# Kernel tuning notes

Measured on AMD Instinct MI355X. Metric: run time of the kernel, lower is better.

## Reference

```python
import jax, jax.numpy as jnp
import numpy as np

N = 100000      # number of nodes
FT = 256        # ft_in (hidden units)
NB_CLASSES = 16 # nb_classes
EPS = 1e-8      # torch.cosine_similarity eps


def setup_inputs() -> dict:
    key = jax.random.key(0)
    ks = jax.random.split(key, 7)
    seq = jax.random.normal(ks[0], (N, FT), dtype=jnp.float32)
    seq1 = jax.random.normal(ks[1], (N, FT), dtype=jnp.float32)
    labels = jax.random.randint(ks[2], (N,), 0, NB_CLASSES, dtype=jnp.int32)
    prompt1 = jax.random.normal(ks[3], (1, FT), dtype=jnp.float32)
    prompt2 = jax.random.normal(ks[4], (1, FT), dtype=jnp.float32)
    prompt3 = jax.random.normal(ks[5], (1, FT), dtype=jnp.float32)
    # weighted_prompt.reset_parameters: fixed init 0.5, 0.4, 0.3
    w_wp = jnp.array([[0.5, 0.4, 0.3]], dtype=jnp.float32)
    # weighted_feature.reset_parameters: fixed init 0.0, 1.0
    w_wf = jnp.array([[0.0, 1.0]], dtype=jnp.float32)
    # downstreamprompt.weight: xavier_uniform on [1, ft_in]
    bound = float(np.sqrt(6.0 / (1 + FT)))
    w_dp = jax.random.uniform(ks[6], (1, FT), jnp.float32, -bound, bound)
    a4 = jnp.array([0.1], dtype=jnp.float32)
    return {"seq": seq, "seq1": seq1, "labels": labels,
            "prompt1": prompt1, "prompt2": prompt2, "prompt3": prompt3,
            "w_wp": w_wp, "w_wf": w_wf, "w_dp": w_dp, "a4": a4}


def reference(seq, seq1, labels, prompt1, prompt2, prompt3, w_wp, w_wf, w_dp, a4):
    # weight = 1 + ELU(weighted_prompt(prompt))  -> [1, FT]
    prompt = jnp.concatenate([prompt1, prompt2, prompt3], axis=0)  # [3, FT]
    weight = 1.0 + jax.nn.elu(w_wp @ prompt)                       # [1, FT]
    rawret1 = weight * seq                                          # [N, FT]
    rawret2 = w_dp * seq                                            # downstreamprompt
    rawret3 = jax.nn.elu(w_wf[0, 0] * rawret1 + w_wf[0, 1] * rawret2)
    rawret = rawret3 + a4[0] * seq1                                 # [N, FT]
    # averageemb (train=1 path): per-class mean, zero-count classes stay 0
    sums = jax.ops.segment_sum(rawret, labels, num_segments=NB_CLASSES)  # [C, FT]
    counts = jax.ops.segment_sum(jnp.ones((rawret.shape[0],), rawret.dtype),
                                 labels, num_segments=NB_CLASSES)        # [C]
    ave = jnp.where(counts[:, None] > 0, sums / jnp.maximum(counts, 1.0)[:, None], sums)
    # fused per-pair cosine similarity: normalize + matmul (replaces N*C loop)
    num = rawret @ ave.T                                             # [N, C]
    denom = (jnp.linalg.norm(rawret, axis=1)[:, None] *
             jnp.linalg.norm(ave, axis=1)[None, :])
    ret = num / jnp.maximum(denom, EPS)
    return jax.nn.softmax(ret, axis=1)
```

## Files before the change

kernel.cpp:

```cpp
#include <hip/hip_runtime.h>
#include <hip/hip_bf16.h>

#define NROWS 100000
#define FT 256
#define NC 16
#define NBLK 512
#define NSL 8
#define SLICE (NBLK / NSL)

#define FPSCALE 1048576.0f
#define FPINV   (1.0f / 1048576.0f)

#define CW_AVEB 0
#define CW_NRM  2048
#define CW_PCNT 2064
#define CW_ST2C (CW_PCNT + NBLK*NC)
#define CW_ST2  (CW_ST2C + NSL*NC)
#define CW_PART (CW_ST2 + NSL*NC*FT)
#define CW_RAWB (CW_PART + NBLK*NC*FT)
#define CW_TOTAL (CW_RAWB + (NROWS*FT)/2)
#define CACHED_NEED_BYTES ((size_t)CW_TOTAL * 4)

#define WS_COEF 0
#define WS_SUMS 256
#define WS_CNTS 4352
#define WS_AVEB 4368
#define WS_NRM  6416

typedef float f32x4 __attribute__((ext_vector_type(4)));
typedef short bf16x8 __attribute__((ext_vector_type(8)));

static __device__ __forceinline__ float bfbits2f(unsigned int u16) {
    union { unsigned int i; float f; } v; v.i = u16 << 16; return v.f;
}
static __device__ __forceinline__ unsigned short f2bf(float f) {
    union { float f; unsigned int i; } v; v.f = f;
    unsigned int u = v.i;
    u += 0x7fffu + ((u >> 16) & 1u);
    return (unsigned short)(u >> 16);
}


__global__ __launch_bounds__(512) void k_accum_c(
    const float* __restrict__ seq,
    const float* __restrict__ seq1,
    const int* __restrict__ labels,
    const float* __restrict__ p1,
    const float* __restrict__ p2,
    const float* __restrict__ p3,
    const float* __restrict__ wwp,
    const float* __restrict__ wwf,
    const float* __restrict__ wdp,
    const float* __restrict__ a4p,
    float* __restrict__ ws)
{
    __shared__ int lsum[NC * FT];
    __shared__ int lcnt[NC];
    __shared__ __align__(16) float scoef[FT];
    const int tid = threadIdx.x;
    for (int i = tid; i < NC * FT; i += 512) lsum[i] = 0;
    if (tid < NC) lcnt[tid] = 0;
    if (tid < FT) {
        float z = wwp[0] * p1[tid] + wwp[1] * p2[tid] + wwp[2] * p3[tid];
        float w = (z > 0.f) ? (1.f + z) : __expf(z);
        scoef[tid] = wwf[0] * w + wwf[1] * wdp[tid];
    }
    __syncthreads();

    const int rr = tid >> 5;
    const int m  = tid & 31;
    const int f0 = m * 8;
    const int mh = m >> 2;
    int off[8];
#pragma unroll
    for (int i = 0; i < 8; ++i) off[i] = (i + mh) & 7;

    float cof[8];
    {
        const float4 c0 = *(const float4*)(scoef + f0);
        const float4 c1 = *(const float4*)(scoef + f0 + 4);
        cof[0]=c0.x; cof[1]=c0.y; cof[2]=c0.z; cof[3]=c0.w;
        cof[4]=c1.x; cof[5]=c1.y; cof[6]=c1.z; cof[7]=c1.w;
    }
    const float a4v = a4p[0];
    unsigned int* rawb = (unsigned int*)(ws + CW_RAWB);

    const int stride = NBLK * 16;
    for (int rowA = blockIdx.x * 16 + rr; rowA < NROWS; rowA += stride * 2) {
        const int rowBr = rowA + stride;
        const bool vB = rowBr < NROWS;
        const int rowB = vB ? rowBr : rowA;
        const int labA = labels[rowA];
        const int labB = labels[rowB];
        const float4 saA = *(const float4*)(seq  + rowA * FT + f0);
        const float4 sbA = *(const float4*)(seq  + rowA * FT + f0 + 4);
        const float4 taA = *(const float4*)(seq1 + rowA * FT + f0);
        const float4 tbA = *(const float4*)(seq1 + rowA * FT + f0 + 4);
        const float4 saB = *(const float4*)(seq  + rowB * FT + f0);
        const float4 sbB = *(const float4*)(seq  + rowB * FT + f0 + 4);
        const float4 taB = *(const float4*)(seq1 + rowB * FT + f0);
        const float4 tbB = *(const float4*)(seq1 + rowB * FT + f0 + 4);

        const float sA[8] = {saA.x,saA.y,saA.z,saA.w, sbA.x,sbA.y,sbA.z,sbA.w};
        const float tA[8] = {taA.x,taA.y,taA.z,taA.w, tbA.x,tbA.y,tbA.z,tbA.w};
        const float sB[8] = {saB.x,saB.y,saB.z,saB.w, sbB.x,sbB.y,sbB.z,sbB.w};
        const float tB[8] = {taB.x,taB.y,taB.z,taB.w, tbB.x,tbB.y,tbB.z,tbB.w};

        int* baseA = lsum + labA * FT + f0;
        unsigned short vbA[8];
#pragma unroll
        for (int i = 0; i < 8; ++i) {
            float u = cof[i] * sA[i];
            float r = (u > 0.f) ? u : (__expf(u) - 1.f);
            float v = r + a4v * tA[i];
            vbA[i] = f2bf(v);
            atomicAdd(baseA + off[i], __float2int_rn(v * FPSCALE));
        }
        uint4 pkA;
        pkA.x = (unsigned int)vbA[0] | ((unsigned int)vbA[1] << 16);
        pkA.y = (unsigned int)vbA[2] | ((unsigned int)vbA[3] << 16);
        pkA.z = (unsigned int)vbA[4] | ((unsigned int)vbA[5] << 16);
        pkA.w = (unsigned int)vbA[6] | ((unsigned int)vbA[7] << 16);
        *(uint4*)(rawb + (rowA * FT + f0) / 2) = pkA;
        if (m == 0) atomicAdd(&lcnt[labA], 1);

        int* baseB = lsum + labB * FT + f0;
        unsigned short vbB[8];
        float vv[8];
#pragma unroll
        for (int i = 0; i < 8; ++i) {
            float u = cof[i] * sB[i];
            float r = (u > 0.f) ? u : (__expf(u) - 1.f);
            vv[i] = r + a4v * tB[i];
            vbB[i] = f2bf(vv[i]);
        }
        if (vB) {
#pragma unroll
            for (int i = 0; i < 8; ++i)
                atomicAdd(baseB + off[i], __float2int_rn(vv[i] * FPSCALE));
            uint4 pkB;
            pkB.x = (unsigned int)vbB[0] | ((unsigned int)vbB[1] << 16);
            pkB.y = (unsigned int)vbB[2] | ((unsigned int)vbB[3] << 16);
            pkB.z = (unsigned int)vbB[4] | ((unsigned int)vbB[5] << 16);
            pkB.w = (unsigned int)vbB[6] | ((unsigned int)vbB[7] << 16);
            *(uint4*)(rawb + (rowB * FT + f0) / 2) = pkB;
            if (m == 0) atomicAdd(&lcnt[labB], 1);
        }
    }
    __syncthreads();

    int* gpart = (int*)(ws + CW_PART) + blockIdx.x * (NC * FT);
    for (int idx = tid; idx < NC * FT; idx += 512) {
        int p  = idx & 255;
        int mm = p >> 3;
        int r  = p & 7;
        int f  = (p & ~7) | ((r - (mm >> 2)) & 7);
        gpart[(idx & ~255) + f] = lsum[idx];
    }
    if (tid < NC) ((int*)(ws + CW_PCNT))[blockIdx.x * NC + tid] = lcnt[tid];
}

__global__ __launch_bounds__(256) void k_reduce1(float* __restrict__ ws)
{
    const int c = blockIdx.x >> 3;
    const int r = blockIdx.x & 7;
    const int f = threadIdx.x;
    const int p0 = r * SLICE;
    const int* gpart = (const int*)(ws + CW_PART);
    int acc = 0;
#pragma unroll 8
    for (int p = 0; p < SLICE; ++p)
        acc += gpart[(p0 + p) * (NC * FT) + c * FT + f];
    ((int*)(ws + CW_ST2))[(r * NC + c) * FT + f] = acc;

    if (f < SLICE) {
        int cc = ((const int*)(ws + CW_PCNT))[(p0 + f) * NC + c];
#pragma unroll
        for (int o = 32; o > 0; o >>= 1) cc += __shfl_down(cc, o, 64);
        if (f == 0) ((int*)(ws + CW_ST2C))[r * NC + c] = cc;
    }
}

__global__ __launch_bounds__(256) void k_reduce2(float* __restrict__ ws)
{
    __shared__ float red[256];
    const int c = blockIdx.x;
    const int f = threadIdx.x;
    const int* st2  = (const int*)(ws + CW_ST2);
    const int* st2c = (const int*)(ws + CW_ST2C);
    long long isum = 0;
    int cnt = 0;
#pragma unroll
    for (int s = 0; s < NSL; ++s) {
        isum += (long long)st2[(s * NC + c) * FT + f];
        cnt  += st2c[s * NC + c];
    }
    float a = ((float)isum * FPINV) / fmaxf((float)cnt, 1.f);
    unsigned short ab = f2bf(a);
    ((unsigned short*)(ws + CW_AVEB))[c * FT + f] = ab;
    float af = bfbits2f(ab);

    red[f] = af * af;
    __syncthreads();
#pragma unroll
    for (int s = 128; s > 0; s >>= 1) {
        if (f < s) red[f] += red[f + s];
        __syncthreads();
    }
    if (f == 0) ws[CW_NRM + c] = sqrtf(red[0]);
}

__global__ __launch_bounds__(256) void k_out_c(
    const float* __restrict__ ws,
    float* __restrict__ out)
{
    const int tid = threadIdx.x;
    const int lane = tid & 63;
    const int wv   = tid >> 6;
    const int c = lane & 15;
    const int g = lane >> 4;

    const unsigned short* aveb = (const unsigned short*)(ws + CW_AVEB);
    const unsigned short* rawb = (const unsigned short*)(ws + CW_RAWB);
    bf16x8 bfrag[8];
#pragma unroll
    for (int kc = 0; kc < 8; ++kc)
        bfrag[kc] = *(const bf16x8*)(aveb + c * FT + kc * 32 + g * 8);
    const float na = ws[CW_NRM + c];

    const int ntiles = NROWS / 16;
    for (int tile = blockIdx.x * 4 + wv; tile < ntiles; tile += gridDim.x * 4) {
        const int rowbase = tile * 16;
        const int arow = rowbase + c;
        f32x4 accC = {0.f, 0.f, 0.f, 0.f};
        f32x4 accS = {0.f, 0.f, 0.f, 0.f};
#pragma unroll
        for (int kc = 0; kc < 8; ++kc) {
            bf16x8 afrag = *(const bf16x8*)(rawb + arow * FT + kc * 32 + g * 8);
            accC = __builtin_amdgcn_mfma_f32_16x16x32_bf16(afrag, bfrag[kc], accC, 0, 0, 0);
            accS = __builtin_amdgcn_mfma_f32_16x16x32_bf16(afrag, afrag,     accS, 0, 0, 0);
        }
#pragma unroll
        for (int q = 0; q < 4; ++q) {
            const float sd = __shfl(accS[q], g * 20 + q, 64);
            const float nr = sqrtf(fmaxf(sd, 0.f));
            const float denom = fmaxf(nr * na, 1e-8f);
            float cosv = accC[q] / denom;
            float mx = cosv;
#pragma unroll
            for (int o = 1; o < 16; o <<= 1) mx = fmaxf(mx, __shfl_xor(mx, o, 16));
            const float e = __expf(cosv - mx);
            float s = e;
#pragma unroll
            for (int o = 1; o < 16; o <<= 1) s += __shfl_xor(s, o, 16);
            out[(rowbase + g * 4 + q) * NC + c] = e / s;
        }
    }
}


__global__ void k_prep(const float* __restrict__ p1,
                       const float* __restrict__ p2,
                       const float* __restrict__ p3,
                       const float* __restrict__ wwp,
                       const float* __restrict__ wwf,
                       const float* __restrict__ wdp,
                       float* __restrict__ ws)
{
    int f = threadIdx.x;
    float z = wwp[0] * p1[f] + wwp[1] * p2[f] + wwp[2] * p3[f];
    float weight = (z > 0.f) ? (1.f + z) : __expf(z);
    ws[WS_COEF + f] = wwf[0] * weight + wwf[1] * wdp[f];
}

__global__ __launch_bounds__(1024) void k_accum(
    const float* __restrict__ seq,
    const float* __restrict__ seq1,
    const int* __restrict__ labels,
    const float* __restrict__ a4p,
    float* __restrict__ ws)
{
    __shared__ int lsum[NC * FT];
    __shared__ int lcnt[NC];
    const int tid = threadIdx.x;
    for (int i = tid; i < NC * FT; i += 1024) lsum[i] = 0;
    if (tid < NC) lcnt[tid] = 0;
    __syncthreads();

    const int rr = tid >> 5;
    const int m  = tid & 31;
    const int f0 = m * 8;
    const int mh = m >> 2;
    int off[8];
#pragma unroll
    for (int i = 0; i < 8; ++i) off[i] = (i + mh) & 7;

    float cof[8];
    {
        const float4 c0 = *(const float4*)(ws + WS_COEF + f0);
        const float4 c1 = *(const float4*)(ws + WS_COEF + f0 + 4);
        cof[0]=c0.x; cof[1]=c0.y; cof[2]=c0.z; cof[3]=c0.w;
        cof[4]=c1.x; cof[5]=c1.y; cof[6]=c1.z; cof[7]=c1.w;
    }
    const float a4v = a4p[0];

    for (int row = blockIdx.x * 32 + rr; row < NROWS; row += gridDim.x * 32) {
        const int lab = labels[row];
        const float4 sa  = *(const float4*)(seq  + row * FT + f0);
        const float4 sb  = *(const float4*)(seq  + row * FT + f0 + 4);
        const float4 ta  = *(const float4*)(seq1 + row * FT + f0);
        const float4 tb  = *(const float4*)(seq1 + row * FT + f0 + 4);
        const float s[8]  = {sa.x,sa.y,sa.z,sa.w, sb.x,sb.y,sb.z,sb.w};
        const float t[8]  = {ta.x,ta.y,ta.z,ta.w, tb.x,tb.y,tb.z,tb.w};
        int* base = lsum + lab * FT + f0;
#pragma unroll
        for (int i = 0; i < 8; ++i) {
            float u = cof[i] * s[i];
            float r = (u > 0.f) ? u : (__expf(u) - 1.f);
            atomicAdd(base + off[i], __float2int_rn((r + a4v * t[i]) * FPSCALE));
        }
        if (m == 0) atomicAdd(&lcnt[lab], 1);
    }
    __syncthreads();

    int* gsum = (int*)(ws + WS_SUMS);
    for (int idx = tid; idx < NC * FT; idx += 1024) {
        int p  = idx & 255;
        int mm = p >> 3;
        int r  = p & 7;
        int f  = (p & ~7) | ((r - (mm >> 2)) & 7);
        atomicAdd(gsum + (idx & ~255) + f, lsum[idx]);
    }
    if (tid < NC) atomicAdd((int*)(ws + WS_CNTS) + tid, lcnt[tid]);
}

__global__ void k_final(float* __restrict__ ws)
{
    __shared__ float nacc[NC];
    const int f = threadIdx.x;
    if (f < NC) nacc[f] = 0.f;
    __syncthreads();
    const int* gsum = (const int*)(ws + WS_SUMS);
    const int* gcnt = (const int*)(ws + WS_CNTS);
    unsigned short* aveb = (unsigned short*)(ws + WS_AVEB);
#pragma unroll
    for (int c = 0; c < NC; ++c) {
        float cnt = (float)gcnt[c];
        float a = ((float)gsum[c * FT + f] * FPINV) / fmaxf(cnt, 1.f);
        unsigned short ab = f2bf(a);
        aveb[c * FT + f] = ab;
        float af = bfbits2f(ab);
        atomicAdd(&nacc[c], af * af);
    }
    __syncthreads();
    if (f < NC) ws[WS_NRM + f] = sqrtf(nacc[f]);
}

__global__ __launch_bounds__(256) void k_out(
    const float* __restrict__ seq,
    const float* __restrict__ seq1,
    const float* __restrict__ a4p,
    const float* __restrict__ ws,
    float* __restrict__ out)
{
    __shared__ __align__(16) float scoef[FT];
    const int tid = threadIdx.x;
    for (int i = tid; i < FT; i += 256) scoef[i] = ws[WS_COEF + i];
    __syncthreads();

    const int lane = tid & 63;
    const int wv   = tid >> 6;
    const int c = lane & 15;
    const int g = lane >> 4;

    const unsigned short* aveb = (const unsigned short*)(ws + WS_AVEB);
    bf16x8 bfrag[8];
#pragma unroll
    for (int kc = 0; kc < 8; ++kc)
        bfrag[kc] = *(const bf16x8*)(aveb + c * FT + kc * 32 + g * 8);
    const float na  = ws[WS_NRM + c];
    const float a4v = a4p[0];

    const int ntiles = NROWS / 16;
    for (int tile = blockIdx.x * 4 + wv; tile < ntiles; tile += gridDim.x * 4) {
        const int rowbase = tile * 16;
        const int arow = rowbase + c;
        f32x4 accC = {0.f, 0.f, 0.f, 0.f};
        f32x4 accS = {0.f, 0.f, 0.f, 0.f};
#pragma unroll
        for (int kc = 0; kc < 8; ++kc) {
            const int k0 = kc * 32 + g * 8;
            const float4 sa = *(const float4*)(seq  + arow * FT + k0);
            const float4 sb = *(const float4*)(seq  + arow * FT + k0 + 4);
            const float4 ta = *(const float4*)(seq1 + arow * FT + k0);
            const float4 tb = *(const float4*)(seq1 + arow * FT + k0 + 4);
            const float4 c0 = *(const float4*)(scoef + k0);
            const float4 c1 = *(const float4*)(scoef + k0 + 4);
            const float s[8]  = {sa.x,sa.y,sa.z,sa.w, sb.x,sb.y,sb.z,sb.w};
            const float t[8]  = {ta.x,ta.y,ta.z,ta.w, tb.x,tb.y,tb.z,tb.w};
            const float cf[8] = {c0.x,c0.y,c0.z,c0.w, c1.x,c1.y,c1.z,c1.w};
            bf16x8 afrag;
#pragma unroll
            for (int i = 0; i < 8; ++i) {
                float u = cf[i] * s[i];
                float r = (u > 0.f) ? u : (__expf(u) - 1.f);
                afrag[i] = (short)f2bf(r + a4v * t[i]);
            }
            accC = __builtin_amdgcn_mfma_f32_16x16x32_bf16(afrag, bfrag[kc], accC, 0, 0, 0);
            accS = __builtin_amdgcn_mfma_f32_16x16x32_bf16(afrag, afrag,     accS, 0, 0, 0);
        }
#pragma unroll
        for (int q = 0; q < 4; ++q) {
            const float sd = __shfl(accS[q], g * 20 + q, 64);
            const float nr = sqrtf(fmaxf(sd, 0.f));
            const float denom = fmaxf(nr * na, 1e-8f);
            float cosv = accC[q] / denom;
            float mx = cosv;
#pragma unroll
            for (int o = 1; o < 16; o <<= 1) mx = fmaxf(mx, __shfl_xor(mx, o, 16));
            const float e = __expf(cosv - mx);
            float s = e;
#pragma unroll
            for (int o = 1; o < 16; o <<= 1) s += __shfl_xor(s, o, 16);
            out[(rowbase + g * 4 + q) * NC + c] = e / s;
        }
    }
}

extern "C" void kernel_launch(void* const* d_in, const int* in_sizes, int n_in,
                              void* d_out, int out_size, void* d_ws, size_t ws_size,
                              hipStream_t stream)
{
    const float* seq  = (const float*)d_in[0];
    const float* seq1 = (const float*)d_in[1];
    const int*   lab  = (const int*)d_in[2];
    const float* p1   = (const float*)d_in[3];
    const float* p2   = (const float*)d_in[4];
    const float* p3   = (const float*)d_in[5];
    const float* wwp  = (const float*)d_in[6];
    const float* wwf  = (const float*)d_in[7];
    const float* wdp  = (const float*)d_in[8];
    const float* a4   = (const float*)d_in[9];
    float* ws  = (float*)d_ws;
    float* out = (float*)d_out;

    if (ws_size >= CACHED_NEED_BYTES) {
        k_accum_c<<<NBLK,     512, 0, stream>>>(seq, seq1, lab, p1, p2, p3,
                                                wwp, wwf, wdp, a4, ws);
        k_reduce1<<<NC * NSL, 256, 0, stream>>>(ws);
        k_reduce2<<<NC,       256, 0, stream>>>(ws);
        k_out_c  <<<1568,     256, 0, stream>>>(ws, out);
    } else {
        hipMemsetAsync((char*)d_ws + WS_SUMS * sizeof(int), 0,
                       (NC * FT + NC) * sizeof(int), stream);
        k_prep <<<1,    256, 0, stream>>>(p1, p2, p3, wwp, wwf, wdp, ws);
        k_accum<<<512, 1024, 0, stream>>>(seq, seq1, lab, a4, ws);
        k_final<<<1,    256, 0, stream>>>(ws);
        k_out  <<<1568, 256, 0, stream>>>(seq, seq1, a4, ws, out);
    }
}
```

Measured before the change: 270.4 us.

## Split fused accumulate kernel into streaming bf16 pass and class-sum pass

The fused kernel, which computed the elementwise transform, wrote bf16 rows and did LDS atomic class sums, is split into two kernels. A pure streaming kernel computes and writes the bf16 rawret. A second 1024-thread kernel rereads the bf16 buffer and does the per-class atomic accumulation. This decouples memory streaming from LDS atomic contention, at the cost of an extra read of the bf16 buffer. Class sums are now built from bf16-rounded values rather than fp32.

```diff
diff --git a/kernel.cpp b/kernel.cpp
--- a/kernel.cpp
+++ b/kernel.cpp
@@ -33,6 +33,9 @@
 static __device__ __forceinline__ float bfbits2f(unsigned int u16) {
     union { unsigned int i; float f; } v; v.i = u16 << 16; return v.f;
 }
+static __device__ __forceinline__ float hi2f(unsigned int u) {
+    union { unsigned int i; float f; } v; v.i = u & 0xffff0000u; return v.f;
+}
 static __device__ __forceinline__ unsigned short f2bf(float f) {
     union { float f; unsigned int i; } v; v.f = f;
     unsigned int u = v.i;
@@ -41,10 +44,9 @@
 }
 
 
-__global__ __launch_bounds__(512) void k_accum_c(
+__global__ __launch_bounds__(256) void k_stream(
     const float* __restrict__ seq,
     const float* __restrict__ seq1,
-    const int* __restrict__ labels,
     const float* __restrict__ p1,
     const float* __restrict__ p2,
     const float* __restrict__ p3,
@@ -54,26 +56,18 @@
     const float* __restrict__ a4p,
     float* __restrict__ ws)
 {
-    __shared__ int lsum[NC * FT];
-    __shared__ int lcnt[NC];
     __shared__ __align__(16) float scoef[FT];
     const int tid = threadIdx.x;
-    for (int i = tid; i < NC * FT; i += 512) lsum[i] = 0;
-    if (tid < NC) lcnt[tid] = 0;
-    if (tid < FT) {
+    {
         float z = wwp[0] * p1[tid] + wwp[1] * p2[tid] + wwp[2] * p3[tid];
         float w = (z > 0.f) ? (1.f + z) : __expf(z);
         scoef[tid] = wwf[0] * w + wwf[1] * wdp[tid];
     }
     __syncthreads();
 
-    const int rr = tid >> 5;
-    const int m  = tid & 31;
-    const int f0 = m * 8;
-    const int mh = m >> 2;
-    int off[8];
-#pragma unroll
-    for (int i = 0; i < 8; ++i) off[i] = (i + mh) & 7;
+    const int S    = gridDim.x * 256;
+    const int gtid = blockIdx.x * 256 + tid;
+    const int f0   = (tid & 31) * 8;
 
     float cof[8];
     {
@@ -85,72 +79,131 @@
     const float a4v = a4p[0];
     unsigned int* rawb = (unsigned int*)(ws + CW_RAWB);
 
-    const int stride = NBLK * 16;
-    for (int rowA = blockIdx.x * 16 + rr; rowA < NROWS; rowA += stride * 2) {
-        const int rowBr = rowA + stride;
+    const int N8 = NROWS * FT / 8;
+    int i = gtid;
+    for (; i + S < N8; i += 2 * S) {
+        const int j = i + S;
+        const float4 sa0 = *(const float4*)(seq  + i * 8);
+        const float4 sb0 = *(const float4*)(seq  + i * 8 + 4);
+        const float4 ta0 = *(const float4*)(seq1 + i * 8);
+        const float4 tb0 = *(const float4*)(seq1 + i * 8 + 4);
+        const float4 sa1 = *(const float4*)(seq  + j * 8);
+        const float4 sb1 = *(const float4*)(seq  + j * 8 + 4);
+        const float4 ta1 = *(const float4*)(seq1 + j * 8);
+        const float4 tb1 = *(const float4*)(seq1 + j * 8 + 4);
+
+        const float s0[8] = {sa0.x,sa0.y,sa0.z,sa0.w, sb0.x,sb0.y,sb0.z,sb0.w};
+        const float t0[8] = {ta0.x,ta0.y,ta0.z,ta0.w, tb0.x,tb0.y,tb0.z,tb0.w};
+        const float s1[8] = {sa1.x,sa1.y,sa1.z,sa1.w, sb1.x,sb1.y,sb1.z,sb1.w};
+        const float t1[8] = {ta1.x,ta1.y,ta1.z,ta1.w, tb1.x,tb1.y,tb1.z,tb1.w};
+
+        unsigned short b0[8], b1[8];
+#pragma unroll
+        for (int k = 0; k < 8; ++k) {
+            float u = cof[k] * s0[k];
+            float r = (u > 0.f) ? u : (__expf(u) - 1.f);
+            b0[k] = f2bf(r + a4v * t0[k]);
+        }
+#pragma unroll
+        for (int k = 0; k < 8; ++k) {
+            float u = cof[k] * s1[k];
+            float r = (u > 0.f) ? u : (__expf(u) - 1.f);
+            b1[k] = f2bf(r + a4v * t1[k]);
+        }
+        uint4 pk0, pk1;
+        pk0.x = (unsigned int)b0[0] | ((unsigned int)b0[1] << 16);
+        pk0.y = (unsigned int)b0[2] | ((unsigned int)b0[3] << 16);
+        pk0.z = (unsigned int)b0[4] | ((unsigned int)b0[5] << 16);
+        pk0.w = (unsigned int)b0[6] | ((unsigned int)b0[7] << 16);
+        pk1.x = (unsigned int)b1[0] | ((unsigned int)b1[1] << 16);
+        pk1.y = (unsigned int)b1[2] | ((unsigned int)b1[3] << 16);
+        pk1.z = (unsigned int)b1[4] | ((unsigned int)b1[5] << 16);
+        pk1.w = (unsigned int)b1[6] | ((unsigned int)b1[7] << 16);
+        *(uint4*)(rawb + i * 4) = pk0;
+        *(uint4*)(rawb + j * 4) = pk1;
+    }
+    for (; i < N8; i += S) {
+        const float4 sa = *(const float4*)(seq  + i * 8);
+        const float4 sb = *(const float4*)(seq  + i * 8 + 4);
+        const float4 ta = *(const float4*)(seq1 + i * 8);
+        const float4 tb = *(const float4*)(seq1 + i * 8 + 4);
+        const float s[8] = {sa.x,sa.y,sa.z,sa.w, sb.x,sb.y,sb.z,sb.w};
+        const float t[8] = {ta.x,ta.y,ta.z,ta.w, tb.x,tb.y,tb.z,tb.w};
+        unsigned short b[8];
+#pragma unroll
+        for (int k = 0; k < 8; ++k) {
+            float u = cof[k] * s[k];
+            float r = (u > 0.f) ? u : (__expf(u) - 1.f);
+            b[k] = f2bf(r + a4v * t[k]);
+        }
+        uint4 pk;
+        pk.x = (unsigned int)b[0] | ((unsigned int)b[1] << 16);
+        pk.y = (unsigned int)b[2] | ((unsigned int)b[3] << 16);
+        pk.z = (unsigned int)b[4] | ((unsigned int)b[5] << 16);
+        pk.w = (unsigned int)b[6] | ((unsigned int)b[7] << 16);
+        *(uint4*)(rawb + i * 4) = pk;
+    }
+}
+
+__global__ __launch_bounds__(1024) void k_csum(
+    const int* __restrict__ labels,
+    float* __restrict__ ws)
+{
+    __shared__ int lsum[NC * FT];
+    __shared__ int lcnt[NC];
+    const int tid = threadIdx.x;
+    for (int i = tid; i < NC * FT; i += 1024) lsum[i] = 0;
+    if (tid < NC) lcnt[tid] = 0;
+    __syncthreads();
+
+    const int rr = tid >> 5;
+    const int m  = tid & 31;
+    const int f0 = m * 8;
+    const int mh = m >> 2;
+    int off[8];
+#pragma unroll
+    for (int i = 0; i < 8; ++i) off[i] = (i + mh) & 7;
+
+    const unsigned int* rawb = (const unsigned int*)(ws + CW_RAWB);
+    const int ST = NBLK * 32;
+
+    for (int rowA = blockIdx.x * 32 + rr; rowA < NROWS; rowA += 2 * ST) {
+        const int rowBr = rowA + ST;
         const bool vB = rowBr < NROWS;
         const int rowB = vB ? rowBr : rowA;
         const int labA = labels[rowA];
         const int labB = labels[rowB];
-        const float4 saA = *(const float4*)(seq  + rowA * FT + f0);
-        const float4 sbA = *(const float4*)(seq  + rowA * FT + f0 + 4);
-        const float4 taA = *(const float4*)(seq1 + rowA * FT + f0);
-        const float4 tbA = *(const float4*)(seq1 + rowA * FT + f0 + 4);
-        const float4 saB = *(const float4*)(seq  + rowB * FT + f0);
-        const float4 sbB = *(const float4*)(seq  + rowB * FT + f0 + 4);
-        const float4 taB = *(const float4*)(seq1 + rowB * FT + f0);
-        const float4 tbB = *(const float4*)(seq1 + rowB * FT + f0 + 4);
-
-        const float sA[8] = {saA.x,saA.y,saA.z,saA.w, sbA.x,sbA.y,sbA.z,sbA.w};
-        const float tA[8] = {taA.x,taA.y,taA.z,taA.w, tbA.x,tbA.y,tbA.z,tbA.w};
-        const float sB[8] = {saB.x,saB.y,saB.z,saB.w, sbB.x,sbB.y,sbB.z,sbB.w};
-        const float tB[8] = {taB.x,taB.y,taB.z,taB.w, tbB.x,tbB.y,tbB.z,tbB.w};
-
+        const uint4 pkA = *(const uint4*)(rawb + (rowA * FT + f0) / 2);
+        const uint4 pkB = *(const uint4*)(rawb + (rowB * FT + f0) / 2);
+
+        const unsigned int ua[4] = {pkA.x, pkA.y, pkA.z, pkA.w};
         int* baseA = lsum + labA * FT + f0;
-        unsigned short vbA[8];
-#pragma unroll
-        for (int i = 0; i < 8; ++i) {
-            float u = cof[i] * sA[i];
-            float r = (u > 0.f) ? u : (__expf(u) - 1.f);
-            float v = r + a4v * tA[i];
-            vbA[i] = f2bf(v);
-            atomicAdd(baseA + off[i], __float2int_rn(v * FPSCALE));
-        }
-        uint4 pkA;
-        pkA.x = (unsigned int)vbA[0] | ((unsigned int)vbA[1] << 16);
-        pkA.y = (unsigned int)vbA[2] | ((unsigned int)vbA[3] << 16);
-        pkA.z = (unsigned int)vbA[4] | ((unsigned int)vbA[5] << 16);
-        pkA.w = (unsigned int)vbA[6] | ((unsigned int)vbA[7] << 16);
-        *(uint4*)(rawb + (rowA * FT + f0) / 2) = pkA;
+#pragma unroll
+        for (int p = 0; p < 4; ++p) {
+            float vlo = bfbits2f(ua[p] & 0xffffu);
+            float vhi = hi2f(ua[p]);
+            atomicAdd(baseA + off[2*p],   __float2int_rn(vlo * FPSCALE));
+            atomicAdd(baseA + off[2*p+1], __float2int_rn(vhi * FPSCALE));
+        }
         if (m == 0) atomicAdd(&lcnt[labA], 1);
 
-        int* baseB = lsum + labB * FT + f0;
-        unsigned short vbB[8];
-        float vv[8];
-#pragma unroll
-        for (int i = 0; i < 8; ++i) {
-            float u = cof[i] * sB[i];
-            float r = (u > 0.f) ? u : (__expf(u) - 1.f);
-            vv[i] = r + a4v * tB[i];
-            vbB[i] = f2bf(vv[i]);
-        }
         if (vB) {
-#pragma unroll
-            for (int i = 0; i < 8; ++i)
-                atomicAdd(baseB + off[i], __float2int_rn(vv[i] * FPSCALE));
-            uint4 pkB;
-            pkB.x = (unsigned int)vbB[0] | ((unsigned int)vbB[1] << 16);
-            pkB.y = (unsigned int)vbB[2] | ((unsigned int)vbB[3] << 16);
-            pkB.z = (unsigned int)vbB[4] | ((unsigned int)vbB[5] << 16);
-            pkB.w = (unsigned int)vbB[6] | ((unsigned int)vbB[7] << 16);
-            *(uint4*)(rawb + (rowB * FT + f0) / 2) = pkB;
+            const unsigned int ub[4] = {pkB.x, pkB.y, pkB.z, pkB.w};
+            int* baseB = lsum + labB * FT + f0;
+#pragma unroll
+            for (int p = 0; p < 4; ++p) {
+                float vlo = bfbits2f(ub[p] & 0xffffu);
+                float vhi = hi2f(ub[p]);
+                atomicAdd(baseB + off[2*p],   __float2int_rn(vlo * FPSCALE));
+                atomicAdd(baseB + off[2*p+1], __float2int_rn(vhi * FPSCALE));
+            }
             if (m == 0) atomicAdd(&lcnt[labB], 1);
         }
     }
     __syncthreads();
 
     int* gpart = (int*)(ws + CW_PART) + blockIdx.x * (NC * FT);
-    for (int idx = tid; idx < NC * FT; idx += 512) {
+    for (int idx = tid; idx < NC * FT; idx += 1024) {
         int p  = idx & 255;
         int mm = p >> 3;
         int r  = p & 7;
@@ -445,8 +498,9 @@
     float* out = (float*)d_out;
 
     if (ws_size >= CACHED_NEED_BYTES) {
-        k_accum_c<<<NBLK,     512, 0, stream>>>(seq, seq1, lab, p1, p2, p3,
-                                                wwp, wwf, wdp, a4, ws);
+        k_stream <<<512,     256, 0, stream>>>(seq, seq1, p1, p2, p3,
+                                               wwp, wwf, wdp, a4, ws);
+        k_csum   <<<NBLK,   1024, 0, stream>>>(lab, ws);
         k_reduce1<<<NC * NSL, 256, 0, stream>>>(ws);
         k_reduce2<<<NC,       256, 0, stream>>>(ws);
         k_out_c  <<<1568,     256, 0, stream>>>(ws, out);
```

Measured after the change: 276.6 us. +2.3%, slower.
